# Performance work log

Hardware: AMD Instinct MI355X
Metric: run time of the kernel (lower is better)

The kernel has to match this reference:

```python
import jax, jax.numpy as jnp
import numpy as np

DIM = 2048
N_HEAD = 32
N_KV_HEAD = 8
HEAD_DIM = DIM // N_HEAD  # 64
BSZ = 2
SEQ = 2048


def apply_rotary_emb(x, freqs_cis):
    # x: [b, s, h, d]; freqs_cis: [s, d//2, 2]
    xs = x.reshape(*x.shape[:-1], -1, 2)          # [b, s, h, d//2, 2]
    fc = freqs_cis.reshape(1, xs.shape[1], 1, xs.shape[3], 2)
    x0, x1 = xs[..., 0], xs[..., 1]
    c, s = fc[..., 0], fc[..., 1]
    out = jnp.stack([x0 * c - x1 * s, x1 * c + x0 * s], axis=-1)
    return out.reshape(x.shape).astype(x.dtype)


def setup_inputs() -> dict:
    key = jax.random.key(0)
    k1, k2, k3, k4 = jax.random.split(key, 4)
    x = jax.random.normal(k1, (BSZ, SEQ, DIM), dtype=jnp.float32)
    # rotary cos/sin table [seq, head_dim//2, 2]
    theta = 1.0 / (10000.0 ** (jnp.arange(0, HEAD_DIM, 2, dtype=jnp.float32) / HEAD_DIM))
    ang = jnp.arange(SEQ, dtype=jnp.float32)[:, None] * theta[None, :]
    freqs_cis = jnp.stack([jnp.cos(ang), jnp.sin(ang)], axis=-1)
    mask = jnp.tril(jnp.ones((SEQ, SEQ), dtype=bool))  # causal
    scale = 0.02
    wqkv = jax.random.normal(k2, ((N_HEAD + 2 * N_KV_HEAD) * HEAD_DIM, DIM), dtype=jnp.float32) * scale
    wo = jax.random.normal(k3, (DIM, DIM), dtype=jnp.float32) * scale
    return {"x": x, "freqs_cis": freqs_cis, "mask": mask, "wqkv": wqkv, "wo": wo}


def reference(x, freqs_cis, mask, wqkv, wo):
    bsz, seqlen, _ = x.shape
    kv_size = N_KV_HEAD * HEAD_DIM
    qkv = x @ wqkv.T  # [b, s, dim + 2*kv]
    xq, xk, xv = jnp.split(qkv, [DIM, DIM + kv_size], axis=-1)
    xq = xq.reshape(bsz, seqlen, N_HEAD, HEAD_DIM)
    xk = xk.reshape(bsz, seqlen, N_KV_HEAD, HEAD_DIM)
    xv = xv.reshape(bsz, seqlen, N_KV_HEAD, HEAD_DIM)
    xq = apply_rotary_emb(xq, freqs_cis)
    xk = apply_rotary_emb(xk, freqs_cis)
    # [b, h, s, d]
    xq = xq.transpose(0, 2, 1, 3)
    xk = xk.transpose(0, 2, 1, 3)
    xv = xv.transpose(0, 2, 1, 3)
    rep = N_HEAD // N_KV_HEAD
    keys = jnp.repeat(xk, rep, axis=1)
    values = jnp.repeat(xv, rep, axis=1)
    scores = jnp.einsum("bhqd,bhkd->bhqk", xq, keys) / np.sqrt(HEAD_DIM).astype(np.float32)
    scores = jnp.where(mask, scores, jnp.finfo(scores.dtype).min)
    attn = jax.nn.softmax(scores, axis=-1)
    out = jnp.einsum("bhqk,bhkd->bhqd", attn, values)
    out = out.transpose(0, 2, 1, 3).reshape(bsz, seqlen, DIM)
    return out @ wo.T
```

## Files before the change

kernel.cpp:

```cpp
#include <hip/hip_runtime.h>
#include <hip/hip_bf16.h>

typedef __attribute__((ext_vector_type(8))) short short8;
typedef __attribute__((ext_vector_type(4))) short short4v;
typedef __attribute__((ext_vector_type(4))) float f32x4;
typedef __hip_bfloat16 bf16;

#define SEQ 2048
#define DIM 2048
#define NH 32
#define NKV 8
#define HD 64
#define QKVD 3072
#define KVD 512
#define SMSCALE 0.18033688011112042f

__device__ inline void gld_lds16(const bf16* g, bf16* l) {
    __builtin_amdgcn_global_load_lds((const __attribute__((address_space(1))) void*)g,
                                     (__attribute__((address_space(3))) void*)l, 16, 0, 0);
}

__device__ inline void store_val(float* p, float v) { *p = v; }
__device__ inline void store_val(bf16* p, float v) { *p = __float2bfloat16(v); }

__device__ inline unsigned pkbf16(float a, float b) {
    __hip_bfloat162 h = __float22bfloat162_rn(make_float2(a, b));
    return *(unsigned*)&h;
}

__device__ inline float b2f(short x) {
    unsigned u = (unsigned)(unsigned short)x << 16;
    union { unsigned u; float f; } c; c.u = u; return c.f;
}

__global__ void cvt3_kernel(const float* __restrict__ x, const float* __restrict__ wqkv,
                            const float* __restrict__ wo, bf16* __restrict__ out) {
    int i = blockIdx.x * blockDim.x + threadIdx.x;
    const float* src; int off;
    if (i < 2097152) { src = x; off = i; }
    else if (i < 3670016) { src = wqkv; off = i - 2097152; }
    else { src = wo; off = i - 3670016; }
    float4 v = ((const float4*)src)[off];
    uint2 u;
    u.x = pkbf16(v.x, v.y);
    u.y = pkbf16(v.z, v.w);
    ((uint2*)out)[i] = u;
}

template <typename CT>
__global__ __launch_bounds__(256, 3) void gemm_nt(const bf16* __restrict__ A,
                                                  const bf16* __restrict__ Bt,
                                                  CT* __restrict__ C,
                                                  int M, int N, int K) {
    __shared__ bf16 As[128 * 32];
    __shared__ bf16 Bs[128 * 32];
    const int tid = threadIdx.x;
    const int lane = tid & 63;
    const int quad = lane >> 4;
    const int r16 = lane & 15;
    const int wave = tid >> 6;
    const int bm = blockIdx.y * 128;
    const int bn = blockIdx.x * 128;
    const int wm = (wave >> 1) * 64;
    const int wn = (wave & 1) * 64;

    f32x4 acc[4][4] = {};

    const int arow = tid >> 2;
    const int kch = (tid & 3) * 8;
    const bf16* Ap = A + (size_t)(bm + arow) * K + kch;
    const bf16* Bp = Bt + (size_t)(bn + arow) * K + kch;
    bf16* Asd = As + tid * 8;
    bf16* Bsd = Bs + tid * 8;
    const int kq = quad * 8;

    for (int k0 = 0; k0 < K; k0 += 32) {
        __syncthreads();
        gld_lds16(Ap, Asd);
        gld_lds16(Ap + (size_t)64 * K, Asd + 64 * 32);
        gld_lds16(Bp, Bsd);
        gld_lds16(Bp + (size_t)64 * K, Bsd + 64 * 32);
        Ap += 32; Bp += 32;
        __syncthreads();
        short8 af[4], bfr[4];
#pragma unroll
        for (int i = 0; i < 4; i++)
            af[i] = *(const short8*)(As + (wm + i * 16 + r16) * 32 + kq);
#pragma unroll
        for (int j = 0; j < 4; j++)
            bfr[j] = *(const short8*)(Bs + (wn + j * 16 + r16) * 32 + kq);
#pragma unroll
        for (int i = 0; i < 4; i++)
#pragma unroll
            for (int j = 0; j < 4; j++)
                acc[i][j] = __builtin_amdgcn_mfma_f32_16x16x32_bf16(af[i], bfr[j], acc[i][j], 0, 0, 0);
    }
#pragma unroll
    for (int i = 0; i < 4; i++)
#pragma unroll
        for (int j = 0; j < 4; j++) {
            int row = bm + wm + i * 16 + quad * 4;
            int col = bn + wn + j * 16 + r16;
#pragma unroll
            for (int r = 0; r < 4; r++)
                store_val(C + (size_t)(row + r) * N + col, acc[i][j][r]);
        }
}

__global__ void rope_qk_kernel(const bf16* __restrict__ qkv, const float* __restrict__ fc,
                               bf16* __restrict__ qr, bf16* __restrict__ kr) {
    const int row = blockIdx.y;
    const int s = row & (SEQ - 1);
    const int col = (blockIdx.x * 64 + threadIdx.x) * 8;
    const bf16* src = qkv + (size_t)row * QKVD + col;
    short8 v = *(const short8*)src;
    const int j0 = (col & 63) >> 1;
    const float4* fcp = (const float4*)(fc + ((size_t)s * 32 + j0) * 2);
    float4 f01 = fcp[0];
    float4 f23 = fcp[1];

    bf16* dst;
    float sc;
    if (col < DIM) { dst = qr + (size_t)row * DIM + col; sc = SMSCALE; }
    else           { dst = kr + (size_t)row * KVD + (col - DIM); sc = 1.0f; }

    float x0 = b2f(v[0]), x1 = b2f(v[1]), x2 = b2f(v[2]), x3 = b2f(v[3]);
    float x4 = b2f(v[4]), x5 = b2f(v[5]), x6 = b2f(v[6]), x7 = b2f(v[7]);
    float c0 = f01.x * sc, s0 = f01.y * sc, c1 = f01.z * sc, s1 = f01.w * sc;
    float c2 = f23.x * sc, s2 = f23.y * sc, c3 = f23.z * sc, s3 = f23.w * sc;

    uint4 o;
    o.x = pkbf16(x0 * c0 - x1 * s0, x1 * c0 + x0 * s0);
    o.y = pkbf16(x2 * c1 - x3 * s1, x3 * c1 + x2 * s1);
    o.z = pkbf16(x4 * c2 - x5 * s2, x5 * c2 + x4 * s2);
    o.w = pkbf16(x6 * c3 - x7 * s3, x7 * c3 + x6 * s3);
    *(uint4*)dst = o;
}

__global__ void rope_v_kernel(const bf16* __restrict__ qkv, bf16* __restrict__ vt) {
    const int t = threadIdx.x;
    const int so = t & 63;
    const int dq = t >> 6;
    const int bk = blockIdx.y;
    const int s = blockIdx.x * 64 + so;
    const int b = bk >> 3;
    const bf16* src = qkv + ((size_t)b * SEQ + s) * QKVD + DIM + KVD + (bk & 7) * HD + dq * 16;
    short8 v0 = *(const short8*)src;
    short8 v1 = *(const short8*)(src + 8);
    short* dst = (short*)(vt + ((size_t)bk * HD + dq * 16) * SEQ + s);
#pragma unroll
    for (int j = 0; j < 8; j++) dst[(size_t)j * SEQ] = v0[j];
#pragma unroll
    for (int j = 0; j < 8; j++) dst[(size_t)(8 + j) * SEQ] = v1[j];
}

__global__ __launch_bounds__(256, 2) void attn_kernel(const bf16* __restrict__ qr,
                                                      const bf16* __restrict__ kr,
                                                      const bf16* __restrict__ vt,
                                                      bf16* __restrict__ out) {
    __shared__ bf16 Ks[8192];
    __shared__ bf16 Vs[8192];
    const int t = threadIdx.x;
    const int lane = t & 63;
    const int wv = t >> 6;
    const int quad = lane >> 4;
    const int r16 = lane & 15;

    const int wg = blockIdx.x;
    const int xcd = wg & 7;
    const int kk = wg >> 3;
    const int bk = xcd * 2 + (kk & 1);
    const int pairIdx = kk >> 1;
    const int b = bk >> 3;
    const int kvh = bk & 7;
    const int h = kvh * 4 + wv;

    const bf16* Kg = kr + ((size_t)b * SEQ + lane) * KVD + kvh * HD + wv * 8;
    const bf16* Vg = vt + ((size_t)(b * NKV + kvh) * HD + lane) * SEQ + wv * 8;

    const char* kl = (const char*)Ks + quad * 1024 + r16 * 16;
    const char* vl = (const char*)Vs + (quad >> 1) * 1024 + r16 * 16 + (quad & 1) * 8;

    union PB { short4v s; unsigned u[2]; };
    const short one_bf16 = (short)0x3F80;
    const short4v ones = {one_bf16, one_bf16, one_bf16, one_bf16};

#pragma unroll 1
    for (int seg = 0; seg < 2; seg++) {
        const int qt = seg ? (63 - pairIdx) : pairIdx;
        const int q0 = qt * 32;
        const int nkb = (qt >> 1) + 1;

        const bf16* QpA = qr + ((size_t)b * SEQ + q0 + r16) * DIM + h * HD + quad * 8;
        const bf16* QpB = QpA + (size_t)16 * DIM;
        short8 qaA0 = *(const short8*)(QpA);
        short8 qaA1 = *(const short8*)(QpA + 32);
        short8 qaB0 = *(const short8*)(QpB);
        short8 qaB1 = *(const short8*)(QpB + 32);

        f32x4 oA[4] = {}, oB[4] = {};
        f32x4 olA = {}, olB = {};

        __syncthreads();
        {
            bf16* Ksd = Ks + t * 8;
            bf16* Vsd = Vs + t * 8;
            gld_lds16(Kg, Ksd);      gld_lds16(Kg + 32, Ksd + 2048);
            gld_lds16(Vg, Vsd);      gld_lds16(Vg + 32, Vsd + 2048);
        }

        for (int kb = 0; kb < nkb; kb++) {
            __syncthreads();
            const int buf = kb & 1;
            if (kb + 1 < nkb) {
                const bf16* Kgn = Kg + (size_t)(kb + 1) * 64 * KVD;
                const bf16* Vgn = Vg + (kb + 1) * 64;
                bf16* Ksd = Ks + (buf ^ 1) * 4096 + t * 8;
                bf16* Vsd = Vs + (buf ^ 1) * 4096 + t * 8;
                gld_lds16(Kgn, Ksd);      gld_lds16(Kgn + 32, Ksd + 2048);
                gld_lds16(Vgn, Vsd);      gld_lds16(Vgn + 32, Vsd + 2048);
            }
            const char* klb = kl + buf * 8192;
            const char* vlb = vl + buf * 8192;

            const f32x4 z = {0.f, 0.f, 0.f, 0.f};
            f32x4 stA[4], stB[4];
            __builtin_amdgcn_s_setprio(1);
#pragma unroll
            for (int n = 0; n < 4; n++) {
                short8 kf0 = *(const short8*)(klb + n * 256);
                short8 kf1 = *(const short8*)(klb + 4096 + n * 256);
                stA[n] = __builtin_amdgcn_mfma_f32_16x16x32_bf16(kf0, qaA0, z, 0, 0, 0);
                stA[n] = __builtin_amdgcn_mfma_f32_16x16x32_bf16(kf1, qaA1, stA[n], 0, 0, 0);
                stB[n] = __builtin_amdgcn_mfma_f32_16x16x32_bf16(kf0, qaB0, z, 0, 0, 0);
                stB[n] = __builtin_amdgcn_mfma_f32_16x16x32_bf16(kf1, qaB1, stB[n], 0, 0, 0);
            }
            __builtin_amdgcn_s_setprio(0);

            short4v vf[4][4];
#pragma unroll
            for (int dt = 0; dt < 4; dt++)
#pragma unroll
                for (int n = 0; n < 4; n++)
                    vf[dt][n] = *(const short4v*)(vlb + n * 2048 + dt * 256);
            __builtin_amdgcn_sched_barrier(0);

            if (kb == nkb - 1) {
                const int kbase = kb * 64;
#pragma unroll
                for (int n = 0; n < 4; n++)
#pragma unroll
                    for (int r = 0; r < 4; r++) {
                        int key = kbase + n * 16 + quad * 4 + r;
                        if (key > q0 + r16) stA[n][r] = -__builtin_inff();
                        if (key > q0 + 16 + r16) stB[n][r] = -__builtin_inff();
                    }
            }

            PB pbsA[4], pbsB[4];
#pragma unroll
            for (int n = 0; n < 4; n++) {
                float a0 = exp2f(stA[n][0]), a1 = exp2f(stA[n][1]);
                float a2 = exp2f(stA[n][2]), a3 = exp2f(stA[n][3]);
                pbsA[n].u[0] = pkbf16(a0, a1);
                pbsA[n].u[1] = pkbf16(a2, a3);
                float b0 = exp2f(stB[n][0]), b1 = exp2f(stB[n][1]);
                float b2 = exp2f(stB[n][2]), b3 = exp2f(stB[n][3]);
                pbsB[n].u[0] = pkbf16(b0, b1);
                pbsB[n].u[1] = pkbf16(b2, b3);
            }

            __builtin_amdgcn_s_setprio(1);
#pragma unroll
            for (int dt = 0; dt < 4; dt++)
#pragma unroll
                for (int n = 0; n < 4; n++) {
                    oA[dt] = __builtin_amdgcn_mfma_f32_16x16x16bf16_1k(vf[dt][n], pbsA[n].s, oA[dt], 0, 0, 0);
                    oB[dt] = __builtin_amdgcn_mfma_f32_16x16x16bf16_1k(vf[dt][n], pbsB[n].s, oB[dt], 0, 0, 0);
                }
#pragma unroll
            for (int n = 0; n < 4; n++) {
                olA = __builtin_amdgcn_mfma_f32_16x16x16bf16_1k(ones, pbsA[n].s, olA, 0, 0, 0);
                olB = __builtin_amdgcn_mfma_f32_16x16x16bf16_1k(ones, pbsB[n].s, olB, 0, 0, 0);
            }
            __builtin_amdgcn_s_setprio(0);
        }

        float invA = 1.f / olA[0];
        float invB = 1.f / olB[0];
        bf16* OpA = out + ((size_t)b * SEQ + q0 + r16) * DIM + h * HD + quad * 4;
        bf16* OpB = OpA + (size_t)16 * DIM;
#pragma unroll
        for (int dt = 0; dt < 4; dt++) {
            PB pka, pkb;
            pka.u[0] = pkbf16(oA[dt][0] * invA, oA[dt][1] * invA);
            pka.u[1] = pkbf16(oA[dt][2] * invA, oA[dt][3] * invA);
            *(short4v*)(OpA + dt * 16) = pka.s;
            pkb.u[0] = pkbf16(oB[dt][0] * invB, oB[dt][1] * invB);
            pkb.u[1] = pkbf16(oB[dt][2] * invB, oB[dt][3] * invB);
            *(short4v*)(OpB + dt * 16) = pkb.s;
        }
    }
}

extern "C" void kernel_launch(void* const* d_in, const int* in_sizes, int n_in,
                              void* d_out, int out_size, void* d_ws, size_t ws_size,
                              hipStream_t stream) {
    (void)in_sizes; (void)n_in; (void)out_size; (void)ws_size;
    const float* x    = (const float*)d_in[0];
    const float* fc   = (const float*)d_in[1];
    const float* wqkv = (const float*)d_in[3];
    const float* wo   = (const float*)d_in[4];
    float* out = (float*)d_out;

    char* w = (char*)d_ws;
    bf16* xb    = (bf16*)(w);
    bf16* wqkvb = (bf16*)(w + 16777216);
    bf16* wob   = (bf16*)(w + 29360128);
    bf16* qkvb  = (bf16*)(w + 37748736);
    bf16* kr    = (bf16*)(w + 62914560);
    bf16* vt    = (bf16*)(w + 67108864);
    bf16* qr = xb;
    bf16* attnb = qkvb;

    cvt3_kernel<<<18432, 256, 0, stream>>>(x, wqkv, wo, xb);
    gemm_nt<bf16><<<dim3(24, 32), 256, 0, stream>>>(xb, wqkvb, qkvb, 4096, QKVD, DIM);
    rope_qk_kernel<<<dim3(5, 4096), 64, 0, stream>>>(qkvb, fc, qr, kr);
    rope_v_kernel<<<dim3(32, 16), 256, 0, stream>>>(qkvb, vt);
    attn_kernel<<<dim3(512), 256, 0, stream>>>(qr, kr, vt, attnb);
    gemm_nt<float><<<dim3(16, 32), 256, 0, stream>>>(attnb, wob, out, 4096, DIM, DIM);
}
```

Baseline: 326.2 us.

## Load K/V fragments directly from global memory instead of LDS staging

Removes the shared-memory double buffer and global-to-LDS async copies for K and V in the attention kernel. Each wave now reads its K and V MFMA fragments straight from global memory into registers at the start of every key block. This drops the block-wide barriers and LDS traffic. In exchange, the four waves redundantly fetch the same K/V through the cache and global load latency is exposed, since there is no prefetch.

```diff
diff --git a/kernel.cpp b/kernel.cpp
--- a/kernel.cpp
+++ b/kernel.cpp
@@ -158,8 +158,6 @@
                                                       const bf16* __restrict__ kr,
                                                       const bf16* __restrict__ vt,
                                                       bf16* __restrict__ out) {
-    __shared__ bf16 Ks[8192];
-    __shared__ bf16 Vs[8192];
     const int t = threadIdx.x;
     const int lane = t & 63;
     const int wv = t >> 6;
@@ -175,11 +173,8 @@
     const int kvh = bk & 7;
     const int h = kvh * 4 + wv;
 
-    const bf16* Kg = kr + ((size_t)b * SEQ + lane) * KVD + kvh * HD + wv * 8;
-    const bf16* Vg = vt + ((size_t)(b * NKV + kvh) * HD + lane) * SEQ + wv * 8;
-
-    const char* kl = (const char*)Ks + quad * 1024 + r16 * 16;
-    const char* vl = (const char*)Vs + (quad >> 1) * 1024 + r16 * 16 + (quad & 1) * 8;
+    const bf16* Kgd = kr + ((size_t)b * SEQ + r16) * KVD + kvh * HD + quad * 8;
+    const bf16* Vgd = vt + ((size_t)(b * NKV + kvh) * HD + r16) * SEQ + quad * 4;
 
     union PB { short4v s; unsigned u[2]; };
     const short one_bf16 = (short)0x3F80;
@@ -201,52 +196,40 @@
         f32x4 oA[4] = {}, oB[4] = {};
         f32x4 olA = {}, olB = {};
 
-        __syncthreads();
-        {
-            bf16* Ksd = Ks + t * 8;
-            bf16* Vsd = Vs + t * 8;
-            gld_lds16(Kg, Ksd);      gld_lds16(Kg + 32, Ksd + 2048);
-            gld_lds16(Vg, Vsd);      gld_lds16(Vg + 32, Vsd + 2048);
-        }
-
+#pragma unroll 1
         for (int kb = 0; kb < nkb; kb++) {
-            __syncthreads();
-            const int buf = kb & 1;
-            if (kb + 1 < nkb) {
-                const bf16* Kgn = Kg + (size_t)(kb + 1) * 64 * KVD;
-                const bf16* Vgn = Vg + (kb + 1) * 64;
-                bf16* Ksd = Ks + (buf ^ 1) * 4096 + t * 8;
-                bf16* Vsd = Vs + (buf ^ 1) * 4096 + t * 8;
-                gld_lds16(Kgn, Ksd);      gld_lds16(Kgn + 32, Ksd + 2048);
-                gld_lds16(Vgn, Vsd);      gld_lds16(Vgn + 32, Vsd + 2048);
-            }
-            const char* klb = kl + buf * 8192;
-            const char* vlb = vl + buf * 8192;
+            const int kbase = kb * 64;
+
+            short8 kfr[4][2];
+            const bf16* Kp = Kgd + (size_t)kbase * KVD;
+#pragma unroll
+            for (int n = 0; n < 4; n++) {
+                kfr[n][0] = *(const short8*)(Kp + (size_t)(n * 16) * KVD);
+                kfr[n][1] = *(const short8*)(Kp + (size_t)(n * 16) * KVD + 32);
+            }
+            short4v vf[4][4];
+#pragma unroll
+            for (int dt = 0; dt < 4; dt++) {
+                const bf16* Vp = Vgd + (size_t)(dt * 16) * SEQ + kbase;
+#pragma unroll
+                for (int n = 0; n < 4; n++)
+                    vf[dt][n] = *(const short4v*)(Vp + n * 16);
+            }
+            __builtin_amdgcn_sched_barrier(0);
 
             const f32x4 z = {0.f, 0.f, 0.f, 0.f};
             f32x4 stA[4], stB[4];
             __builtin_amdgcn_s_setprio(1);
 #pragma unroll
             for (int n = 0; n < 4; n++) {
-                short8 kf0 = *(const short8*)(klb + n * 256);
-                short8 kf1 = *(const short8*)(klb + 4096 + n * 256);
-                stA[n] = __builtin_amdgcn_mfma_f32_16x16x32_bf16(kf0, qaA0, z, 0, 0, 0);
-                stA[n] = __builtin_amdgcn_mfma_f32_16x16x32_bf16(kf1, qaA1, stA[n], 0, 0, 0);
-                stB[n] = __builtin_amdgcn_mfma_f32_16x16x32_bf16(kf0, qaB0, z, 0, 0, 0);
-                stB[n] = __builtin_amdgcn_mfma_f32_16x16x32_bf16(kf1, qaB1, stB[n], 0, 0, 0);
+                stA[n] = __builtin_amdgcn_mfma_f32_16x16x32_bf16(kfr[n][0], qaA0, z, 0, 0, 0);
+                stA[n] = __builtin_amdgcn_mfma_f32_16x16x32_bf16(kfr[n][1], qaA1, stA[n], 0, 0, 0);
+                stB[n] = __builtin_amdgcn_mfma_f32_16x16x32_bf16(kfr[n][0], qaB0, z, 0, 0, 0);
+                stB[n] = __builtin_amdgcn_mfma_f32_16x16x32_bf16(kfr[n][1], qaB1, stB[n], 0, 0, 0);
             }
             __builtin_amdgcn_s_setprio(0);
 
-            short4v vf[4][4];
-#pragma unroll
-            for (int dt = 0; dt < 4; dt++)
-#pragma unroll
-                for (int n = 0; n < 4; n++)
-                    vf[dt][n] = *(const short4v*)(vlb + n * 2048 + dt * 256);
-            __builtin_amdgcn_sched_barrier(0);
-
             if (kb == nkb - 1) {
-                const int kbase = kb * 64;
 #pragma unroll
                 for (int n = 0; n < 4; n++)
 #pragma unroll
```

Measured after the change: 425.1 us. +30.3%, slower.

## Triple-buffer K/V tiles in attention with explicit vmcnt waits

Applied to the files above, without the earlier changes.

Replaces the double-buffered K/V LDS staging in the attention kernel with a three-stage ring. Tiles are prefetched two iterations ahead, and explicit s_waitcnt vmcnt counts plus raw s_barrier replace __syncthreads, so loads stay in flight across iterations. The aim is to hide global-to-LDS latency better. In exchange, LDS use grows from 32KB to 48KB per block, which may limit occupancy with two blocks per CU.

```diff
diff --git a/kernel.cpp b/kernel.cpp
--- a/kernel.cpp
+++ b/kernel.cpp
@@ -158,8 +158,8 @@
                                                       const bf16* __restrict__ kr,
                                                       const bf16* __restrict__ vt,
                                                       bf16* __restrict__ out) {
-    __shared__ bf16 Ks[8192];
-    __shared__ bf16 Vs[8192];
+    __shared__ bf16 Ks[3 * 4096];
+    __shared__ bf16 Vs[3 * 4096];
     const int t = threadIdx.x;
     const int lane = t & 63;
     const int wv = t >> 6;
@@ -185,6 +185,14 @@
     const short one_bf16 = (short)0x3F80;
     const short4v ones = {one_bf16, one_bf16, one_bf16, one_bf16};
 
+#define STAGE(tile, sbuf) {                                        \
+        const bf16* Kgn = Kg + (size_t)(tile) * 64 * KVD;          \
+        const bf16* Vgn = Vg + (tile) * 64;                        \
+        bf16* Ksd = Ks + (sbuf) * 4096 + t * 8;                    \
+        bf16* Vsd = Vs + (sbuf) * 4096 + t * 8;                    \
+        gld_lds16(Kgn, Ksd);  gld_lds16(Kgn + 32, Ksd + 2048);     \
+        gld_lds16(Vgn, Vsd);  gld_lds16(Vgn + 32, Vsd + 2048); }
+
 #pragma unroll 1
     for (int seg = 0; seg < 2; seg++) {
         const int qt = seg ? (63 - pairIdx) : pairIdx;
@@ -197,31 +205,35 @@
         short8 qaA1 = *(const short8*)(QpA + 32);
         short8 qaB0 = *(const short8*)(QpB);
         short8 qaB1 = *(const short8*)(QpB + 32);
+        __builtin_amdgcn_sched_barrier(0);
+
+        asm volatile("s_waitcnt vmcnt(0)" ::: "memory");
 
         f32x4 oA[4] = {}, oB[4] = {};
         f32x4 olA = {}, olB = {};
 
-        __syncthreads();
-        {
-            bf16* Ksd = Ks + t * 8;
-            bf16* Vsd = Vs + t * 8;
-            gld_lds16(Kg, Ksd);      gld_lds16(Kg + 32, Ksd + 2048);
-            gld_lds16(Vg, Vsd);      gld_lds16(Vg + 32, Vsd + 2048);
-        }
-
+        __builtin_amdgcn_s_barrier();
+        __builtin_amdgcn_sched_barrier(0);
+
+        STAGE(0, 0);
+        if (nkb > 1) STAGE(1, 1);
+
+        int cb = 0;
+        int sb = 2;
+
+#pragma unroll 1
         for (int kb = 0; kb < nkb; kb++) {
-            __syncthreads();
-            const int buf = kb & 1;
-            if (kb + 1 < nkb) {
-                const bf16* Kgn = Kg + (size_t)(kb + 1) * 64 * KVD;
-                const bf16* Vgn = Vg + (kb + 1) * 64;
-                bf16* Ksd = Ks + (buf ^ 1) * 4096 + t * 8;
-                bf16* Vsd = Vs + (buf ^ 1) * 4096 + t * 8;
-                gld_lds16(Kgn, Ksd);      gld_lds16(Kgn + 32, Ksd + 2048);
-                gld_lds16(Vgn, Vsd);      gld_lds16(Vgn + 32, Vsd + 2048);
-            }
-            const char* klb = kl + buf * 8192;
-            const char* vlb = vl + buf * 8192;
+            if (kb == nkb - 1) { asm volatile("s_waitcnt vmcnt(0)" ::: "memory"); }
+            else               { asm volatile("s_waitcnt vmcnt(4)" ::: "memory"); }
+            __builtin_amdgcn_sched_barrier(0);
+            __builtin_amdgcn_s_barrier();
+            __builtin_amdgcn_sched_barrier(0);
+
+            if (kb + 2 < nkb) STAGE(kb + 2, sb);
+
+            const char* klb = kl + cb * 8192;
+            const char* vlb = vl + cb * 8192;
+            const int kbase = kb * 64;
 
             const f32x4 z = {0.f, 0.f, 0.f, 0.f};
             f32x4 stA[4], stB[4];
@@ -246,7 +258,6 @@
             __builtin_amdgcn_sched_barrier(0);
 
             if (kb == nkb - 1) {
-                const int kbase = kb * 64;
 #pragma unroll
                 for (int n = 0; n < 4; n++)
 #pragma unroll
@@ -284,6 +295,9 @@
                 olB = __builtin_amdgcn_mfma_f32_16x16x16bf16_1k(ones, pbsB[n].s, olB, 0, 0, 0);
             }
             __builtin_amdgcn_s_setprio(0);
+
+            cb = (cb == 2) ? 0 : cb + 1;
+            sb = (sb == 2) ? 0 : sb + 1;
         }
 
         float invA = 1.f / olA[0];
@@ -301,6 +315,7 @@
             *(short4v*)(OpB + dt * 16) = pkb.s;
         }
     }
+#undef STAGE
 }
 
 extern "C" void kernel_launch(void* const* d_in, const int* in_sizes, int n_in,
```

Result: no change. 322.4 us (-1.2%).
